# Performance work log

Hardware: AMD Instinct MI355X
Metric: run time of the kernel (lower is better)

## Reference

```python
import jax, jax.numpy as jnp
import numpy as np

N_LAYERS, D_MODEL, H, D_K, D_V, D_FF, VOCAB = 6, 512, 8, 64, 64, 2048, 32000
B, S = 4, 512
NEG_INF = -jnp.inf


def positional_encoding(seq_len, d_model):
    # Faithful to the (buggy-vs-paper) source: angle = pos / 10000**(2*i/d_model),
    # sin for even i, cos for odd i (i is the raw channel index).
    pos = jnp.arange(seq_len, dtype=jnp.float32)[:, None]
    i = jnp.arange(d_model, dtype=jnp.float32)[None, :]
    angle = pos / jnp.power(10000.0, 2.0 * i / d_model)
    return jnp.where((jnp.arange(d_model) % 2 == 0)[None, :], jnp.sin(angle), jnp.cos(angle))


def layer_norm(x, g, b, eps=1e-5):
    mu = jnp.mean(x, -1, keepdims=True)
    var = jnp.mean((x - mu) ** 2, -1, keepdims=True)
    return (x - mu) * jax.lax.rsqrt(var + eps) * g + b


def mha(q_in, k_in, v_in, wq, wk, wv, wo, q_mask, k_mask, causal):
    # wq/wk: (H, D, D_K), wv: (H, D, D_V), wo: (H*D_V, D)
    q = jnp.einsum('bsd,hdk->bhsk', q_in, wq)
    k = jnp.einsum('btd,hdk->bhtk', k_in, wk)
    v = jnp.einsum('btd,hdk->bhtk', v_in, wv)
    scores = jnp.einsum('bhsk,bhtk->bhst', q, k) / jnp.sqrt(jnp.float32(D_K))
    allowed = q_mask[:, None, :, None] & k_mask[:, None, None, :]  # (B,1,S,T)
    if causal:
        sl, tl = q_in.shape[1], k_in.shape[1]
        allowed = allowed & (jnp.arange(tl)[None, :] <= jnp.arange(sl)[:, None])[None, None]
    scores = jnp.where(allowed, scores, NEG_INF)
    attn = jax.nn.softmax(scores, axis=-1)
    out = jnp.einsum('bhst,bhtk->bshk', attn, v)  # (B,S,H,D_V)
    out = out.reshape(out.shape[0], out.shape[1], H * D_V)
    return out @ wo


def ffn(x, w1, b1, w2, b2):
    return jax.nn.relu(x @ w1 + b1) @ w2 + b2


def setup_inputs() -> dict:
    key = jax.random.key(0)
    ks = iter(jax.random.split(key, 40))
    f = lambda shape, scale: (jax.random.normal(next(ks), shape, dtype=jnp.float32) * scale)
    inp = {
        'src_tokens': jax.random.randint(next(ks), (B, S), 0, VOCAB),
        'tgt_tokens': jax.random.randint(next(ks), (B, S), 0, VOCAB),
        'src_mask': jnp.ones((B, S), dtype=bool),
        'tgt_mask': jnp.ones((B, S), dtype=bool),
        'embed': f((VOCAB, D_MODEL), 0.02),
        'enc_wqkv': f((N_LAYERS, 3, H, D_MODEL, D_K), 0.04),
        'enc_wo': f((N_LAYERS, H * D_V, D_MODEL), 0.04),
        'enc_ff_w1': f((N_LAYERS, D_MODEL, D_FF), 0.02),
        'enc_ff_b1': jnp.zeros((N_LAYERS, D_FF), jnp.float32),
        'enc_ff_w2': f((N_LAYERS, D_FF, D_MODEL), 0.02),
        'enc_ff_b2': jnp.zeros((N_LAYERS, D_MODEL), jnp.float32),
        'enc_ln_g': jnp.ones((N_LAYERS, 2, D_MODEL), jnp.float32),
        'enc_ln_b': jnp.zeros((N_LAYERS, 2, D_MODEL), jnp.float32),
        'dec_wqkv1': f((N_LAYERS, 3, H, D_MODEL, D_K), 0.04),
        'dec_wo1': f((N_LAYERS, H * D_V, D_MODEL), 0.04),
        'dec_wqkv2': f((N_LAYERS, 3, H, D_MODEL, D_K), 0.04),
        'dec_wo2': f((N_LAYERS, H * D_V, D_MODEL), 0.04),
        'dec_ff_w1': f((N_LAYERS, D_MODEL, D_FF), 0.02),
        'dec_ff_b1': jnp.zeros((N_LAYERS, D_FF), jnp.float32),
        'dec_ff_w2': f((N_LAYERS, D_FF, D_MODEL), 0.02),
        'dec_ff_b2': jnp.zeros((N_LAYERS, D_MODEL), jnp.float32),
        'dec_ln_g': jnp.ones((N_LAYERS, 3, D_MODEL), jnp.float32),
        'dec_ln_b': jnp.zeros((N_LAYERS, 3, D_MODEL), jnp.float32),
        'out_w': f((D_MODEL, VOCAB), 0.02),
        'out_b': jnp.zeros((VOCAB,), jnp.float32),
    }
    return inp


def reference(src_tokens, tgt_tokens, src_mask, tgt_mask, embed,
              enc_wqkv, enc_wo, enc_ff_w1, enc_ff_b1, enc_ff_w2, enc_ff_b2, enc_ln_g, enc_ln_b,
              dec_wqkv1, dec_wo1, dec_wqkv2, dec_wo2, dec_ff_w1, dec_ff_b1, dec_ff_w2, dec_ff_b2,
              dec_ln_g, dec_ln_b, out_w, out_b):
    pe = positional_encoding(src_tokens.shape[1], D_MODEL)
    x = embed[src_tokens] + pe[None]
    for i in range(N_LAYERS):
        a = mha(x, x, x, enc_wqkv[i, 0], enc_wqkv[i, 1], enc_wqkv[i, 2], enc_wo[i], src_mask, src_mask, False)
        x = layer_norm(x + a, enc_ln_g[i, 0], enc_ln_b[i, 0])
        x = layer_norm(x + ffn(x, enc_ff_w1[i], enc_ff_b1[i], enc_ff_w2[i], enc_ff_b2[i]), enc_ln_g[i, 1], enc_ln_b[i, 1])
    pe_t = positional_encoding(tgt_tokens.shape[1], D_MODEL)
    y = embed[tgt_tokens] + pe_t[None]
    for i in range(N_LAYERS):
        a = mha(y, y, y, dec_wqkv1[i, 0], dec_wqkv1[i, 1], dec_wqkv1[i, 2], dec_wo1[i], tgt_mask, tgt_mask, True)
        y = layer_norm(y + a, dec_ln_g[i, 0], dec_ln_b[i, 0])
        a = mha(y, x, x, dec_wqkv2[i, 0], dec_wqkv2[i, 1], dec_wqkv2[i, 2], dec_wo2[i], tgt_mask, src_mask, False)
        y = layer_norm(y + a, dec_ln_g[i, 1], dec_ln_b[i, 1])
        y = layer_norm(y + ffn(y, dec_ff_w1[i], dec_ff_b1[i], dec_ff_w2[i], dec_ff_b2[i]), dec_ln_g[i, 2], dec_ln_b[i, 2])
    return y @ out_w + out_b
```

## Files before the change

### kernel.cpp

```cpp
#include <hip/hip_runtime.h>
#include <math.h>


typedef unsigned short u16;
typedef __attribute__((ext_vector_type(8))) short short8;
typedef __attribute__((ext_vector_type(4))) float f32x4;

__device__ __forceinline__ u16 f2bf(float f){
  unsigned u = __float_as_uint(f);
  return (u16)((u + 0x7fffu + ((u >> 16) & 1u)) >> 16);
}

#define GLDS16(gp, lp) __builtin_amdgcn_global_load_lds( \
    (const __attribute__((address_space(1))) unsigned int*)(const void*)(gp), \
    (__attribute__((address_space(3))) unsigned int*)(void*)(lp), 16, 0, 0)

__global__ __launch_bounds__(256) void embed_dual_kernel(
    const int* __restrict__ src, const int* __restrict__ tgt,
    const float* __restrict__ emb,
    float* __restrict__ xb, u16* __restrict__ xh,
    float* __restrict__ yb, u16* __restrict__ yh)
{
  int which = blockIdx.x >> 11;
  int row = blockIdx.x & 2047;
  int s = row & 511;
  int t = which ? tgt[row] : src[row];
  float* out = which ? yb : xb;
  u16*  outh = which ? yh : xh;
  #pragma unroll
  for (int j = 0; j < 2; j++){
    int d = threadIdx.x + 256*j;
    float ang = (float)s * powf(10000.0f, -2.0f*(float)d/512.0f);
    float pe = (d & 1) ? cosf(ang) : sinf(ang);
    float v = emb[(size_t)t*512 + d] + pe;
    out[(size_t)row*512 + d] = v;
    outh[(size_t)row*512 + d] = f2bf(v);
  }
}

struct WDesc { const float* W; unsigned long long gs, ds; u16* dst; int K; int nx; int end; };
struct WPack { WDesc d[6]; };

__device__ __forceinline__ void cast_body(const WPack& P, int nseg, int blk){
  __shared__ u16 T[64][65];
  int s = 0;
  while (s < nseg-1 && blk >= P.d[s].end) s++;
  WDesc D = P.d[s];
  int base = s ? P.d[s-1].end : 0;
  int lb = blk - base;
  int g = lb % D.nx, kt = lb / D.nx;
  int tid = threadIdx.x;
  const float* Wb = D.W + (size_t)g*D.gs + (size_t)kt*64*D.ds;
  #pragma unroll
  for (int i = 0; i < 16; i++){
    int li = tid + 256*i;
    int kk = li >> 6, c = li & 63;
    T[kk][c] = f2bf(Wb[(size_t)kk*D.ds + c]);
  }
  __syncthreads();
  #pragma unroll
  for (int i = 0; i < 16; i++){
    int lo = tid + 256*i;
    int c = lo >> 6, kk = lo & 63;
    D.dst[(size_t)(g*64 + c)*D.K + kt*64 + kk] = T[kk][c];
  }
}

__global__ __launch_bounds__(256) void wcast_multi(WPack P, int nseg){
  cast_body(P, nseg, blockIdx.x);
}

__device__ __forceinline__ void ln_body(
    float* __restrict__ x, const float* __restrict__ res,
    const float* __restrict__ g, const float* __restrict__ bt,
    u16* __restrict__ xh, int blk)
{
  int tid = threadIdx.x, lane = tid & 63, wv = tid >> 6;
  int row = blk*4 + wv;
  size_t base = (size_t)row*512;
  float v[8]; float sum = 0.f;
  #pragma unroll
  for (int j = 0; j < 8; j++){
    int d = lane + 64*j;
    v[j] = x[base + d] + res[base + d];
    sum += v[j];
  }
  #pragma unroll
  for (int o = 32; o; o >>= 1) sum += __shfl_xor(sum, o);
  float mu = sum * (1.0f/512.0f);
  float vs = 0.f;
  #pragma unroll
  for (int j = 0; j < 8; j++){ float dd = v[j] - mu; vs += dd*dd; }
  #pragma unroll
  for (int o = 32; o; o >>= 1) vs += __shfl_xor(vs, o);
  float rstd = rsqrtf(vs*(1.0f/512.0f) + 1e-5f);
  #pragma unroll
  for (int j = 0; j < 8; j++){
    int d = lane + 64*j;
    float ov = (v[j] - mu)*rstd*g[d] + bt[d];
    x[base + d] = ov;
    xh[base + d] = f2bf(ov);
  }
}

__global__ __launch_bounds__(256) void ln_cast_kernel(
    float* __restrict__ x, const float* __restrict__ res,
    const float* __restrict__ g, const float* __restrict__ bt,
    u16* __restrict__ xh, WPack P, int nseg)
{
  int bid = blockIdx.x;
  if (bid < 512){ ln_body(x, res, g, bt, xh, bid); return; }
  cast_body(P, nseg, bid - 512);
}

__global__ __launch_bounds__(256) void ln_kernel(
    float* __restrict__ x, const float* __restrict__ res,
    const float* __restrict__ g, const float* __restrict__ bt,
    u16* __restrict__ xh)
{
  ln_body(x, res, g, bt, xh, blockIdx.x);
}

__global__ __launch_bounds__(512) void flash_attn_kernel(
    const u16* __restrict__ qkv, const u16* __restrict__ vT,
    u16* __restrict__ ctx, int causal)
{
  __shared__ __align__(16) u16 lQ[64*64];
  __shared__ __align__(16) u16 lK[4][64*64];
  __shared__ __align__(16) u16 lV[4][64*64];
  __shared__ __align__(16) u16 lP[8][16*64];
  int tid = threadIdx.x, lane = tid & 63, w = tid >> 6;
  int g = w >> 2, wl = w & 3;
  int r16 = lane & 15, l4 = lane >> 4;
  int bh = blockIdx.x >> 3, qb = blockIdx.x & 7;
  int b = bh >> 3, h = bh & 7;
  const u16* qbase = qkv + (size_t)b*512*1536 + h*64;
  int sr = tid >> 3, sc = tid & 7;

  GLDS16(qbase + (size_t)(qb*64 + sr)*1536 + ((sc ^ (sr & 7))*8),
         lQ + (w << 6)*8);
  auto stageK = [&](int buf, int tt){
    GLDS16(qbase + 512 + (size_t)(tt*64 + sr)*1536 + ((sc ^ (sr & 7))*8),
           lK[buf] + (w << 6)*8);
  };
  auto stageV = [&](int buf, int tt){
    GLDS16(vT + ((size_t)bh*64 + sr)*512 + tt*64 + ((sc ^ (sr & 7))*8),
           lV[buf] + (w << 6)*8);
  };

  int ntl = causal ? (qb + 1) : 8;
  int nrounds = (ntl + 1) >> 1;
  stageK(0, 0); stageV(0, 0);
  if (ntl > 1){ stageK(1, 1); stageV(1, 1); }
  __syncthreads();

  short8 qa[2];
  #pragma unroll
  for (int kt = 0; kt < 2; kt++){
    int q = wl*16 + r16;
    qa[kt] = *(const short8*)&lQ[q*64 + (((kt*4 + l4) ^ (q & 7))*8)];
  }

  f32x4 o[4];
  float mrow[4], lrow[4];
  #pragma unroll
  for (int j = 0; j < 4; j++){ o[j] = (f32x4){0.f,0.f,0.f,0.f}; mrow[j] = -3e38f; lrow[j] = 0.f; }

  for (int rd = 0; rd < nrounds; rd++){
    if (rd > 0) __syncthreads();
    if (rd + 1 < nrounds){
      int base = ((rd + 1) & 1)*2;
      int t0 = 2*(rd + 1);
      stageK(base, t0); stageV(base, t0);
      if (t0 + 1 < ntl){ stageK(base + 1, t0 + 1); stageV(base + 1, t0 + 1); }
    }
    int tr = 2*rd + g;
    if (tr < ntl){
      int buf = (rd & 1)*2 + g;
      f32x4 s[4];
      #pragma unroll
      for (int ct = 0; ct < 4; ct++) s[ct] = (f32x4){0.f,0.f,0.f,0.f};
      __builtin_amdgcn_s_setprio(1);
      #pragma unroll
      for (int kt = 0; kt < 2; kt++){
        #pragma unroll
        for (int ct = 0; ct < 4; ct++){
          int trow = ct*16 + r16;
          short8 kb = *(const short8*)&lK[buf][trow*64 + (((kt*4 + l4) ^ (trow & 7))*8)];
          s[ct] = __builtin_amdgcn_mfma_f32_16x16x32_bf16(qa[kt], kb, s[ct], 0, 0, 0);
        }
      }
      __builtin_amdgcn_s_setprio(0);
      float p[4][4];
      #pragma unroll
      for (int ct = 0; ct < 4; ct++)
        #pragma unroll
        for (int r = 0; r < 4; r++){
          float v = s[ct][r] * 0.125f;
          if (causal && tr == qb && (ct*16 + r16) > (wl*16 + l4*4 + r)) v = -1e30f;
          p[ct][r] = v;
        }
      #pragma unroll
      for (int r = 0; r < 4; r++){
        float pm = fmaxf(fmaxf(p[0][r], p[1][r]), fmaxf(p[2][r], p[3][r]));
        #pragma unroll
        for (int off = 1; off < 16; off <<= 1) pm = fmaxf(pm, __shfl_xor(pm, off));
        float mn = fmaxf(mrow[r], pm);
        float scl = __expf(mrow[r] - mn);
        mrow[r] = mn;
        float rs = 0.f;
        #pragma unroll
        for (int ct = 0; ct < 4; ct++){ p[ct][r] = __expf(p[ct][r] - mn); rs += p[ct][r]; }
        #pragma unroll
        for (int off = 1; off < 16; off <<= 1) rs += __shfl_xor(rs, off);
        lrow[r] = lrow[r]*scl + rs;
        #pragma unroll
        for (int jf = 0; jf < 4; jf++) o[jf][r] *= scl;
      }
      u16* myP = &lP[w][0];
      #pragma unroll
      for (int ct = 0; ct < 4; ct++)
        #pragma unroll
        for (int r = 0; r < 4; r++){
          int q = l4*4 + r, t = ct*16 + r16;
          myP[q*64 + (((t >> 3) ^ (q & 7))*8) + (t & 7)] = f2bf(p[ct][r]);
        }
      __builtin_amdgcn_s_setprio(1);
      #pragma unroll
      for (int kt = 0; kt < 2; kt++){
        short8 pa = *(const short8*)&myP[r16*64 + (((kt*4 + l4) ^ (r16 & 7))*8)];
        #pragma unroll
        for (int jf = 0; jf < 4; jf++){
          int dr = jf*16 + r16;
          short8 vv = *(const short8*)&lV[buf][dr*64 + (((kt*4 + l4) ^ (dr & 7))*8)];
          o[jf] = __builtin_amdgcn_mfma_f32_16x16x32_bf16(pa, vv, o[jf], 0, 0, 0);
        }
      }
      __builtin_amdgcn_s_setprio(0);
    }
  }

  __syncthreads();
  float* mrg = (float*)&lK[0][0];
  if (w >= 4){
    float* p = mrg + ((size_t)(wl*64 + lane))*25;
    #pragma unroll
    for (int r = 0; r < 4; r++){ p[r] = mrow[r]; p[4 + r] = lrow[r]; }
    #pragma unroll
    for (int jf = 0; jf < 4; jf++)
      #pragma unroll
      for (int r = 0; r < 4; r++) p[8 + jf*4 + r] = o[jf][r];
  }
  __syncthreads();
  if (w < 4){
    float* p = mrg + ((size_t)(w*64 + lane))*25;
    #pragma unroll
    for (int r = 0; r < 4; r++){
      float m1 = p[r], l1 = p[4 + r];
      float M  = fmaxf(mrow[r], m1);
      float s0 = __expf(mrow[r] - M), s1 = __expf(m1 - M);
      float L  = lrow[r]*s0 + l1*s1;
      float inv = 1.0f / L;
      int q = qb*64 + w*16 + l4*4 + r;
      u16* dst = ctx + (size_t)(b*512 + q)*512 + h*64;
      #pragma unroll
      for (int jf = 0; jf < 4; jf++)
        dst[jf*16 + r16] = f2bf((o[jf][r]*s0 + p[8 + jf*4 + r]*s1) * inv);
    }
  }
}

template<int BM, int BN, int WM, int WN, int WK, int VOUT, int SWZ>
__global__ __launch_bounds__(WM*WN*WK*64) void mfma_gemm(
    const u16* __restrict__ A, int lda,
    const u16* __restrict__ B, int ldb,
    void* __restrict__ C, int ldc, int cbf,
    const float* __restrict__ bias, int relu, int K, u16* __restrict__ vt)
{
  constexpr int NWC = WM*WN;
  constexpr int NT  = NWC*WK*64;
  constexpr int TPS = NWC*64;
  constexpr int SM  = BM/WM, SN = BN/WN;
  constexpr int FM  = SM/16, FN = SN/16;
  constexpr int RPS = TPS/8;
  constexpr int AG  = BM/RPS, BG = BN/RPS;
  __shared__ __align__(16) u16 lds[2][WK][(BM+BN)*64];
  int bx, by;
  if constexpr (SWZ){
    int nwg = gridDim.x * gridDim.y;
    int lin = blockIdx.y * gridDim.x + blockIdx.x;
    int q = nwg >> 3, r = nwg & 7;
    int xcd = lin & 7, idx = lin >> 3;
    int wgid = (xcd < r ? xcd*(q+1) : r*(q+1) + (xcd-r)*q) + idx;
    bx = wgid / gridDim.y; by = wgid % gridDim.y;
  } else { bx = blockIdx.x; by = blockIdx.y; }
  int tid = threadIdx.x, lane = tid & 63, w = tid >> 6;
  int wk = w / NWC, wl = w % NWC;
  int wm = wl / WN, wn = wl % WN;
  int r16 = lane & 15, l4 = lane >> 4;
  int stid = tid % TPS, slc = tid / TPS;
  int ws = stid >> 6;
  int sr = stid >> 3, sc = stid & 7;
  int scs = sc ^ (sr & 7);
  int kslc = K/WK;
  const u16* Ab = A + (size_t)by*BM*lda + (size_t)sr*lda + scs*8 + (size_t)slc*kslc;
  const u16* Bb = B + (size_t)bx*BN*ldb + (size_t)sr*ldb + scs*8 + (size_t)slc*kslc;
  f32x4 acc[FM][FN];
  #pragma unroll
  for (int i = 0; i < FM; i++)
    #pragma unroll
    for (int j = 0; j < FN; j++)
      acc[i][j] = (f32x4){0.f, 0.f, 0.f, 0.f};

  auto stage = [&](int buf, int kt){
    #pragma unroll
    for (int s = 0; s < AG; s++)
      GLDS16(Ab + (size_t)(s*RPS)*lda + kt, &lds[buf][slc][(s*RPS + (ws << 3))*64]);
    #pragma unroll
    for (int s = 0; s < BG; s++)
      GLDS16(Bb + (size_t)(s*RPS)*ldb + kt, &lds[buf][slc][(BM + s*RPS + (ws << 3))*64]);
  };
  stage(0, 0);
  int nk = kslc >> 6, cur = 0;
  for (int kt = 0; kt < nk; kt++){
    __syncthreads();
    if (kt + 1 < nk) stage(cur ^ 1, (kt + 1) << 6);
    #pragma unroll
    for (int ks = 0; ks < 2; ks++){
      short8 av[FM], bv[FN];
      #pragma unroll
      for (int i = 0; i < FM; i++){
        int row = wm*SM + i*16 + r16;
        av[i] = *(const short8*)&lds[cur][wk][row*64 + (((ks*4 + l4) ^ (row & 7))*8)];
      }
      #pragma unroll
      for (int j = 0; j < FN; j++){
        int row = wn*SN + j*16 + r16;
        bv[j] = *(const short8*)&lds[cur][wk][(BM + row)*64 + (((ks*4 + l4) ^ (row & 7))*8)];
      }
      #pragma unroll
      for (int i = 0; i < FM; i++)
        #pragma unroll
        for (int j = 0; j < FN; j++)
          acc[i][j] = __builtin_amdgcn_mfma_f32_16x16x32_bf16(av[i], bv[j], acc[i][j], 0, 0, 0);
    }
    cur ^= 1;
  }

  if constexpr (WK == 2){
    __syncthreads();
    float* Mg = (float*)&lds[0][0][0];
    if (wk == 1){
      #pragma unroll
      for (int i = 0; i < FM; i++)
        #pragma unroll
        for (int j = 0; j < FN; j++)
          #pragma unroll
          for (int r = 0; r < 4; r++)
            Mg[(size_t)(wm*SM + i*16 + l4*4 + r)*(BN + 4) + wn*SN + j*16 + r16]
                = acc[i][j][r];
    }
    __syncthreads();
    if (wk == 0){
      #pragma unroll
      for (int i = 0; i < FM; i++)
        #pragma unroll
        for (int j = 0; j < FN; j++)
          #pragma unroll
          for (int r = 0; r < 4; r++)
            acc[i][j][r] += Mg[(size_t)(wm*SM + i*16 + l4*4 + r)*(BN + 4)
                               + wn*SN + j*16 + r16];
    }
  }

  if constexpr (VOUT){
    int nblk = bx * BN;
    if (nblk >= 1024){
      constexpr int TP = BM + 4;
      u16* T = &lds[0][0][0];
      __syncthreads();
      if (wk == 0){
        #pragma unroll
        for (int i = 0; i < FM; i++){
          int t0 = wm*SM + i*16 + l4*4;
          #pragma unroll
          for (int j = 0; j < FN; j++){
            int d = wn*SN + j*16 + r16;
            unsigned q01 = (unsigned)f2bf(acc[i][j][0]) | ((unsigned)f2bf(acc[i][j][1]) << 16);
            unsigned q23 = (unsigned)f2bf(acc[i][j][2]) | ((unsigned)f2bf(acc[i][j][3]) << 16);
            uint2 pk; pk.x = q01; pk.y = q23;
            *(uint2*)&T[d*TP + t0] = pk;
          }
        }
      }
      __syncthreads();
      int h0 = (nblk - 1024) >> 6;
      int b = (by * BM) >> 9;
      int t0g = (by * BM) & 511;
      constexpr int U2PR = BM/4;
      constexpr int NIT = (BN*BM)/(NT*4);
      #pragma unroll
      for (int it = 0; it < NIT; it++){
        int idx = it*NT + tid;
        int d = idx / U2PR, tq = (idx % U2PR)*4;
        int hh = d >> 6, dd = d & 63;
        *(uint2*)&vt[((size_t)((b*8 + h0 + hh)*64 + dd))*512 + t0g + tq] =
            *(const uint2*)&T[d*TP + tq];
      }
      return;
    }
  }

  if (wk != 0) return;
  int m0 = by*BM + wm*SM, n0 = bx*BN + wn*SN;
  int r4 = l4*4;
  #pragma unroll
  for (int i = 0; i < FM; i++){
    #pragma unroll
    for (int j = 0; j < FN; j++){
      int col = n0 + j*16 + r16;
      float bi = bias ? bias[col] : 0.f;
      #pragma unroll
      for (int r = 0; r < 4; r++){
        int rowg = m0 + i*16 + r4 + r;
        float o = acc[i][j][r] + bi;
        if (relu) o = fmaxf(o, 0.f);
        if (cbf) ((u16*)C)[(size_t)rowg*ldc + col] = f2bf(o);
        else     ((float*)C)[(size_t)rowg*ldc + col] = o;
      }
    }
  }
}

__global__ __launch_bounds__(256) void xattn_qkv_gemm(
    const u16* __restrict__ Ay, const u16* __restrict__ Ax,
    const u16* __restrict__ Bt, u16* __restrict__ C, u16* __restrict__ vt)
{
  constexpr int BM=64, BN=64, WM=2, WN=2, NT=256;
  constexpr int SM=BM/WM, SN=BN/WN, FM=SM/16, FN=SN/16, RPS=NT/8;
  constexpr int AG=BM/RPS, BG=BN/RPS;
  __shared__ __align__(16) u16 lA[2][BM*64];
  __shared__ __align__(16) u16 lB[2][BN*64];
  int tid = threadIdx.x, lane = tid & 63, w = tid >> 6;
  int wm = w / WN, wn = w % WN;
  int r16 = lane & 15, l4 = lane >> 4;
  int sr = (w << 3) + (lane >> 3);
  int sc = lane & 7;
  int scs = sc ^ (sr & 7);
  int z = blockIdx.z;
  const u16* A = (z == 0) ? Ay : Ax;
  const u16* Ab = A + (size_t)blockIdx.y*BM*512 + (size_t)sr*512 + scs*8;
  const u16* Bb = Bt + (size_t)(z*512 + blockIdx.x*BN)*512 + (size_t)sr*512 + scs*8;
  f32x4 acc[FM][FN];
  #pragma unroll
  for (int i = 0; i < FM; i++)
    #pragma unroll
    for (int j = 0; j < FN; j++)
      acc[i][j] = (f32x4){0.f, 0.f, 0.f, 0.f};
  auto stage = [&](int buf, int kt){
    #pragma unroll
    for (int s = 0; s < AG; s++)
      GLDS16(Ab + (size_t)(s*RPS)*512 + kt, &lA[buf][(s*RPS + (w << 3))*64]);
    #pragma unroll
    for (int s = 0; s < BG; s++)
      GLDS16(Bb + (size_t)(s*RPS)*512 + kt, &lB[buf][(s*RPS + (w << 3))*64]);
  };
  stage(0, 0);
  int cur = 0;
  for (int kt = 0; kt < 8; kt++){
    __syncthreads();
    if (kt + 1 < 8) stage(cur ^ 1, (kt + 1) << 6);
    #pragma unroll
    for (int ks = 0; ks < 2; ks++){
      short8 av[FM], bv[FN];
      #pragma unroll
      for (int i = 0; i < FM; i++){
        int row = wm*SM + i*16 + r16;
        av[i] = *(const short8*)&lA[cur][row*64 + (((ks*4 + l4) ^ (row & 7))*8)];
      }
      #pragma unroll
      for (int j = 0; j < FN; j++){
        int row = wn*SN + j*16 + r16;
        bv[j] = *(const short8*)&lB[cur][row*64 + (((ks*4 + l4) ^ (row & 7))*8)];
      }
      #pragma unroll
      for (int i = 0; i < FM; i++)
        #pragma unroll
        for (int j = 0; j < FN; j++)
          acc[i][j] = __builtin_amdgcn_mfma_f32_16x16x32_bf16(av[i], bv[j], acc[i][j], 0, 0, 0);
    }
    cur ^= 1;
  }
  if (z == 2){
    constexpr int TP = BM + 4;
    u16* T = (u16*)&lA[0][0];
    __syncthreads();
    #pragma unroll
    for (int i = 0; i < FM; i++){
      int t0 = wm*SM + i*16 + l4*4;
      #pragma unroll
      for (int j = 0; j < FN; j++){
        int d = wn*SN + j*16 + r16;
        unsigned q01 = (unsigned)f2bf(acc[i][j][0]) | ((unsigned)f2bf(acc[i][j][1]) << 16);
        unsigned q23 = (unsigned)f2bf(acc[i][j][2]) | ((unsigned)f2bf(acc[i][j][3]) << 16);
        uint2 pk; pk.x = q01; pk.y = q23;
        *(uint2*)&T[d*TP + t0] = pk;
      }
    }
    __syncthreads();
    int h = blockIdx.x;
    int b = (blockIdx.y * BM) >> 9;
    int t0g = (blockIdx.y * BM) & 511;
    u16* dst = vt + (size_t)(b*8 + h)*64*512;
    #pragma unroll
    for (int it = 0; it < (BM*64)/(NT*4); it++){
      int idx = it*NT + tid;
      int d = idx >> 4, tq = (idx & 15)*4;
      *(uint2*)&dst[(size_t)d*512 + t0g + tq] = *(const uint2*)&T[d*TP + tq];
    }
    return;
  }
  int m0 = blockIdx.y*BM + wm*SM, n0 = z*512 + blockIdx.x*BN + wn*SN;
  int r4 = l4*4;
  #pragma unroll
  for (int i = 0; i < FM; i++)
    #pragma unroll
    for (int j = 0; j < FN; j++)
      #pragma unroll
      for (int r = 0; r < 4; r++){
        int rowg = m0 + i*16 + r4 + r;
        C[(size_t)rowg*1536 + n0 + j*16 + r16] = f2bf(acc[i][j][r]);
      }
}

extern "C" void kernel_launch(void* const* d_in, const int* in_sizes, int n_in,
                              void* d_out, int out_size, void* d_ws, size_t ws_size,
                              hipStream_t stream)
{
  (void)in_sizes; (void)n_in; (void)out_size; (void)ws_size;
  const int*   src_tok   = (const int*)  d_in[0];
  const int*   tgt_tok   = (const int*)  d_in[1];
  const float* emb       = (const float*)d_in[4];
  const float* enc_wqkv  = (const float*)d_in[5];
  const float* enc_wo    = (const float*)d_in[6];
  const float* enc_ff_w1 = (const float*)d_in[7];
  const float* enc_ff_b1 = (const float*)d_in[8];
  const float* enc_ff_w2 = (const float*)d_in[9];
  const float* enc_ff_b2 = (const float*)d_in[10];
  const float* enc_ln_g  = (const float*)d_in[11];
  const float* enc_ln_b  = (const float*)d_in[12];
  const float* dec_wqkv1 = (const float*)d_in[13];
  const float* dec_wo1   = (const float*)d_in[14];
  const float* dec_wqkv2 = (const float*)d_in[15];
  const float* dec_wo2   = (const float*)d_in[16];
  const float* dec_ff_w1 = (const float*)d_in[17];
  const float* dec_ff_b1 = (const float*)d_in[18];
  const float* dec_ff_w2 = (const float*)d_in[19];
  const float* dec_ff_b2 = (const float*)d_in[20];
  const float* dec_ln_g  = (const float*)d_in[21];
  const float* dec_ln_b  = (const float*)d_in[22];
  const float* out_w     = (const float*)d_in[23];
  const float* out_b     = (const float*)d_in[24];
  float* outp = (float*)d_out;

  const size_t MB = 1024*1024;
  char* wsb = (char*)d_ws;
  float* xb     = (float*)(wsb + 0*MB);
  u16*   sQKV2  = (u16*)  (wsb + 0*MB);
  u16*   sWO2   = (u16*)  (wsb + 1*MB + 512*1024);
  float* yb     = (float*)(wsb + 4*MB);
  u16*   xh     = (u16*)  (wsb + 8*MB);
  u16*   ctxb   = (u16*)  (wsb + 10*MB);
  u16*   yh     = (u16*)  (wsb + 12*MB);
  u16*   qkvb   = (u16*)  (wsb + 14*MB);
  u16*   vT     = (u16*)  (wsb + 20*MB);
  u16*   hid    = (u16*)  (wsb + 14*MB);
  u16*   sQKV   = (u16*)  (wsb + 22*MB);
  u16*   sWO    = (u16*)  (wsb + 23*MB + 512*1024);
  u16*   sFF1   = (u16*)  (wsb + 24*MB);
  u16*   sFF2   = (u16*)  (wsb + 26*MB);
  float* proj   = (float*)(wsb + 28*MB);
  u16*   wvbuf  = (u16*)  (wsb + 14*MB);

  auto g64 = [&](const u16* A,int lda,const u16* B,int ldb,void* C,int ldc,
                 int cbf,const float* bias,int relu,int M,int N,int K){
    mfma_gemm<64,64,2,2,2,0,0><<<dim3(N/64, M/64), 512, 0, stream>>>(
        A,lda,B,ldb,C,ldc,cbf,bias,relu,K,nullptr);
  };
  auto g128 = [&](const u16* A,int lda,const u16* B,int ldb,void* C,int ldc,
                  int cbf,const float* bias,int relu,int M,int N,int K){
    mfma_gemm<128,128,2,2,2,0,0><<<dim3(N/128, M/128), 512, 0, stream>>>(
        A,lda,B,ldb,C,ldc,cbf,bias,relu,K,nullptr);
  };
  auto gvocab = [&](const u16* A,const u16* B,void* C,int ldc,
                    const float* bias,int N){
    mfma_gemm<128,64,2,2,1,0,1><<<dim3(N/64, 16), 256, 0, stream>>>(
        A,512,B,512,C,ldc,0,bias,0,512,nullptr);
  };
  auto gqkv = [&](const u16* A,const u16* B,u16* C,u16* vt){
    mfma_gemm<128,128,2,2,2,1,0><<<dim3(12, 16), 512, 0, stream>>>(
        A,512,B,512,C,1536,1,nullptr,0,512,vt);
  };
  auto ln = [&](float* x, const float* g, const float* b, u16* oh){
    ln_kernel<<<512, 256, 0, stream>>>(x, proj, g, b, oh);
  };
  auto packof = [&](WDesc* segs, int n, int& tot){
    WPack P; tot = 0;
    for (int s = 0; s < n; s++){
      tot += segs[s].nx * (segs[s].K/64);
      segs[s].end = tot;
      P.d[s] = segs[s];
    }
    for (int s = n; s < 6; s++) P.d[s] = P.d[0];
    return P;
  };
  auto cast = [&](WDesc* segs, int n){
    int tot; WPack P = packof(segs, n, tot);
    wcast_multi<<<tot, 256, 0, stream>>>(P, n);
  };
  auto ln_cast = [&](float* x, const float* g, const float* b, u16* oh,
                     WDesc* segs, int n){
    int tot; WPack P = packof(segs, n, tot);
    ln_cast_kernel<<<512 + tot, 256, 0, stream>>>(x, proj, g, b, oh, P, n);
  };

  const size_t WQKV_L = (size_t)3*8*512*64;
  auto enc_segs = [&](int i, WDesc* s){
    s[0] = {enc_wqkv + i*WQKV_L,            32768, 64,   sQKV, 512,  24, 0};
    s[1] = {enc_wo   + (size_t)i*262144,    64,    512,  sWO,  512,  8,  0};
    s[2] = {enc_ff_w1+ (size_t)i*512*2048,  64,    2048, sFF1, 512,  32, 0};
    s[3] = {enc_ff_w2+ (size_t)i*2048*512,  64,    512,  sFF2, 2048, 8,  0};
  };
  auto dec_segs = [&](int i, WDesc* s){
    s[0] = {dec_wqkv1 + i*WQKV_L,           32768, 64,   sQKV,  512,  24, 0};
    s[1] = {dec_wo1   + (size_t)i*262144,   64,    512,  sWO,   512,  8,  0};
    s[2] = {dec_ff_w1 + (size_t)i*512*2048, 64,    2048, sFF1,  512,  32, 0};
    s[3] = {dec_ff_w2 + (size_t)i*2048*512, 64,    512,  sFF2,  2048, 8,  0};
    s[4] = {dec_wqkv2 + i*WQKV_L,           32768, 64,   sQKV2, 512,  24, 0};
    s[5] = {dec_wo2   + (size_t)i*262144,   64,    512,  sWO2,  512,  8,  0};
  };

  embed_dual_kernel<<<4096, 256, 0, stream>>>(src_tok, tgt_tok, emb, xb, xh, yb, yh);

  { WDesc s[4]; enc_segs(0, s); cast(s, 4); }
  for (int i = 0; i < 6; i++){
    gqkv(xh, sQKV, qkvb, vT);
    flash_attn_kernel<<<256, 512, 0, stream>>>(qkvb, vT, ctxb, 0);
    g64(ctxb, 512, sWO, 512, proj, 512, 0, nullptr, 0, 2048, 512, 512);
    ln(xb, enc_ln_g + i*1024, enc_ln_b + i*1024, xh);
    g128(xh, 512, sFF1, 512, hid, 2048, 1, enc_ff_b1 + i*2048, 1, 2048, 2048, 512);
    g64(hid, 2048, sFF2, 2048, proj, 512, 0, enc_ff_b2 + i*512, 0, 2048, 512, 2048);
    if (i < 5){
      WDesc s[4]; enc_segs(i+1, s);
      ln_cast(xb, enc_ln_g + i*1024 + 512, enc_ln_b + i*1024 + 512, xh, s, 4);
    } else {
      ln(xb, enc_ln_g + i*1024 + 512, enc_ln_b + i*1024 + 512, xh);
    }
  }

  { WDesc s[6]; dec_segs(0, s); cast(s, 6); }
  for (int i = 0; i < 6; i++){
    gqkv(yh, sQKV, qkvb, vT);
    flash_attn_kernel<<<256, 512, 0, stream>>>(qkvb, vT, ctxb, 1);
    g64(ctxb, 512, sWO, 512, proj, 512, 0, nullptr, 0, 2048, 512, 512);
    ln(yb, dec_ln_g + i*1536,        dec_ln_b + i*1536,        yh);
    xattn_qkv_gemm<<<dim3(8, 32, 3), 256, 0, stream>>>(yh, xh, sQKV2, qkvb, vT);
    flash_attn_kernel<<<256, 512, 0, stream>>>(qkvb, vT, ctxb, 0);
    g64(ctxb, 512, sWO2, 512, proj, 512, 0, nullptr, 0, 2048, 512, 512);
    ln(yb, dec_ln_g + i*1536 + 512,  dec_ln_b + i*1536 + 512,  yh);
    g128(yh, 512, sFF1, 512, hid, 2048, 1, dec_ff_b1 + i*2048, 1, 2048, 2048, 512);
    g64(hid, 2048, sFF2, 2048, proj, 512, 0, dec_ff_b2 + i*512, 0, 2048, 512, 2048);
    if (i < 5){
      WDesc s[6]; dec_segs(i+1, s);
      ln_cast(yb, dec_ln_g + i*1536 + 1024, dec_ln_b + i*1536 + 1024, yh, s, 6);
    } else {
      ln(yb, dec_ln_g + i*1536 + 1024, dec_ln_b + i*1536 + 1024, yh);
    }
  }

  for (int c = 0; c < 2; c++){
    int c0 = c*16000;
    WDesc seg[1] = {{out_w + c0, 64, 32000, wvbuf, 512, 250, 0}};
    cast(seg, 1);
    gvocab(yh, wvbuf, outp + c0, 32000, out_b + c0, 16000);
  }
}
```

Baseline: 1.298 ms.

## Split-K across two warp groups in cross-attn QKV GEMM; share Q/P LDS in flash attention

```diff
diff --git a/kernel.cpp b/kernel.cpp
--- a/kernel.cpp
+++ b/kernel.cpp
@@ -125,10 +125,9 @@
     const u16* __restrict__ qkv, const u16* __restrict__ vT,
     u16* __restrict__ ctx, int causal)
 {
-  __shared__ __align__(16) u16 lQ[64*64];
+  __shared__ __align__(16) u16 lQP[8*16*64];
   __shared__ __align__(16) u16 lK[4][64*64];
   __shared__ __align__(16) u16 lV[4][64*64];
-  __shared__ __align__(16) u16 lP[8][16*64];
   int tid = threadIdx.x, lane = tid & 63, w = tid >> 6;
   int g = w >> 2, wl = w & 3;
   int r16 = lane & 15, l4 = lane >> 4;
@@ -138,7 +137,7 @@
   int sr = tid >> 3, sc = tid & 7;
 
   GLDS16(qbase + (size_t)(qb*64 + sr)*1536 + ((sc ^ (sr & 7))*8),
-         lQ + (w << 6)*8);
+         lQP + (w << 6)*8);
   auto stageK = [&](int buf, int tt){
     GLDS16(qbase + 512 + (size_t)(tt*64 + sr)*1536 + ((sc ^ (sr & 7))*8),
            lK[buf] + (w << 6)*8);
@@ -158,8 +157,9 @@
   #pragma unroll
   for (int kt = 0; kt < 2; kt++){
     int q = wl*16 + r16;
-    qa[kt] = *(const short8*)&lQ[q*64 + (((kt*4 + l4) ^ (q & 7))*8)];
-  }
+    qa[kt] = *(const short8*)&lQP[q*64 + (((kt*4 + l4) ^ (q & 7))*8)];
+  }
+  __syncthreads();
 
   f32x4 o[4];
   float mrow[4], lrow[4];
@@ -217,7 +217,7 @@
         #pragma unroll
         for (int jf = 0; jf < 4; jf++) o[jf][r] *= scl;
       }
-      u16* myP = &lP[w][0];
+      u16* myP = &lQP[w*16*64];
       #pragma unroll
       for (int ct = 0; ct < 4; ct++)
         #pragma unroll
@@ -432,25 +432,28 @@
   }
 }
 
-__global__ __launch_bounds__(256) void xattn_qkv_gemm(
+__global__ __launch_bounds__(512) void xattn_qkv_gemm(
     const u16* __restrict__ Ay, const u16* __restrict__ Ax,
     const u16* __restrict__ Bt, u16* __restrict__ C, u16* __restrict__ vt)
 {
-  constexpr int BM=64, BN=64, WM=2, WN=2, NT=256;
-  constexpr int SM=BM/WM, SN=BN/WN, FM=SM/16, FN=SN/16, RPS=NT/8;
+  constexpr int BM=64, BN=64, WM=2, WN=2, WK=2;
+  constexpr int NWC=WM*WN, NT=NWC*WK*64, TPS=NWC*64;
+  constexpr int SM=BM/WM, SN=BN/WN, FM=SM/16, FN=SN/16, RPS=TPS/8;
   constexpr int AG=BM/RPS, BG=BN/RPS;
-  __shared__ __align__(16) u16 lA[2][BM*64];
-  __shared__ __align__(16) u16 lB[2][BN*64];
+  __shared__ __align__(16) u16 lds[2][WK][(BM+BN)*64];
   int tid = threadIdx.x, lane = tid & 63, w = tid >> 6;
-  int wm = w / WN, wn = w % WN;
+  int wk = w / NWC, wl = w % NWC;
+  int wm = wl / WN, wn = wl % WN;
   int r16 = lane & 15, l4 = lane >> 4;
-  int sr = (w << 3) + (lane >> 3);
-  int sc = lane & 7;
+  int stid = tid % TPS, slc = tid / TPS;
+  int ws = stid >> 6;
+  int sr = stid >> 3, sc = stid & 7;
   int scs = sc ^ (sr & 7);
   int z = blockIdx.z;
   const u16* A = (z == 0) ? Ay : Ax;
-  const u16* Ab = A + (size_t)blockIdx.y*BM*512 + (size_t)sr*512 + scs*8;
-  const u16* Bb = Bt + (size_t)(z*512 + blockIdx.x*BN)*512 + (size_t)sr*512 + scs*8;
+  const u16* Ab = A + (size_t)blockIdx.y*BM*512 + (size_t)sr*512 + scs*8 + (size_t)slc*256;
+  const u16* Bb = Bt + (size_t)(z*512 + blockIdx.x*BN)*512 + (size_t)sr*512 + scs*8
+                  + (size_t)slc*256;
   f32x4 acc[FM][FN];
   #pragma unroll
   for (int i = 0; i < FM; i++)
@@ -460,28 +463,28 @@
   auto stage = [&](int buf, int kt){
     #pragma unroll
     for (int s = 0; s < AG; s++)
-      GLDS16(Ab + (size_t)(s*RPS)*512 + kt, &lA[buf][(s*RPS + (w << 3))*64]);
+      GLDS16(Ab + (size_t)(s*RPS)*512 + kt, &lds[buf][slc][(s*RPS + (ws << 3))*64]);
     #pragma unroll
     for (int s = 0; s < BG; s++)
-      GLDS16(Bb + (size_t)(s*RPS)*512 + kt, &lB[buf][(s*RPS + (w << 3))*64]);
+      GLDS16(Bb + (size_t)(s*RPS)*512 + kt, &lds[buf][slc][(BM + s*RPS + (ws << 3))*64]);
   };
   stage(0, 0);
   int cur = 0;
-  for (int kt = 0; kt < 8; kt++){
+  for (int kt = 0; kt < 4; kt++){
     __syncthreads();
-    if (kt + 1 < 8) stage(cur ^ 1, (kt + 1) << 6);
+    if (kt + 1 < 4) stage(cur ^ 1, (kt + 1) << 6);
     #pragma unroll
     for (int ks = 0; ks < 2; ks++){
       short8 av[FM], bv[FN];
       #pragma unroll
       for (int i = 0; i < FM; i++){
         int row = wm*SM + i*16 + r16;
-        av[i] = *(const short8*)&lA[cur][row*64 + (((ks*4 + l4) ^ (row & 7))*8)];
+        av[i] = *(const short8*)&lds[cur][wk][row*64 + (((ks*4 + l4) ^ (row & 7))*8)];
       }
       #pragma unroll
       for (int j = 0; j < FN; j++){
         int row = wn*SN + j*16 + r16;
-        bv[j] = *(const short8*)&lB[cur][row*64 + (((ks*4 + l4) ^ (row & 7))*8)];
+        bv[j] = *(const short8*)&lds[cur][wk][(BM + row)*64 + (((ks*4 + l4) ^ (row & 7))*8)];
       }
       #pragma unroll
       for (int i = 0; i < FM; i++)
@@ -491,20 +494,45 @@
     }
     cur ^= 1;
   }
+  __syncthreads();
+  float* Mg = (float*)&lds[0][0][0];
+  if (wk == 1){
+    #pragma unroll
+    for (int i = 0; i < FM; i++)
+      #pragma unroll
+      for (int j = 0; j < FN; j++)
+        #pragma unroll
+        for (int r = 0; r < 4; r++)
+          Mg[(size_t)(wm*SM + i*16 + l4*4 + r)*(BN + 4) + wn*SN + j*16 + r16]
+              = acc[i][j][r];
+  }
+  __syncthreads();
+  if (wk == 0){
+    #pragma unroll
+    for (int i = 0; i < FM; i++)
+      #pragma unroll
+      for (int j = 0; j < FN; j++)
+        #pragma unroll
+        for (int r = 0; r < 4; r++)
+          acc[i][j][r] += Mg[(size_t)(wm*SM + i*16 + l4*4 + r)*(BN + 4)
+                             + wn*SN + j*16 + r16];
+  }
   if (z == 2){
     constexpr int TP = BM + 4;
-    u16* T = (u16*)&lA[0][0];
+    u16* T = &lds[0][0][0];
     __syncthreads();
-    #pragma unroll
-    for (int i = 0; i < FM; i++){
-      int t0 = wm*SM + i*16 + l4*4;
-      #pragma unroll
-      for (int j = 0; j < FN; j++){
-        int d = wn*SN + j*16 + r16;
-        unsigned q01 = (unsigned)f2bf(acc[i][j][0]) | ((unsigned)f2bf(acc[i][j][1]) << 16);
-        unsigned q23 = (unsigned)f2bf(acc[i][j][2]) | ((unsigned)f2bf(acc[i][j][3]) << 16);
-        uint2 pk; pk.x = q01; pk.y = q23;
-        *(uint2*)&T[d*TP + t0] = pk;
+    if (wk == 0){
+      #pragma unroll
+      for (int i = 0; i < FM; i++){
+        int t0 = wm*SM + i*16 + l4*4;
+        #pragma unroll
+        for (int j = 0; j < FN; j++){
+          int d = wn*SN + j*16 + r16;
+          unsigned q01 = (unsigned)f2bf(acc[i][j][0]) | ((unsigned)f2bf(acc[i][j][1]) << 16);
+          unsigned q23 = (unsigned)f2bf(acc[i][j][2]) | ((unsigned)f2bf(acc[i][j][3]) << 16);
+          uint2 pk; pk.x = q01; pk.y = q23;
+          *(uint2*)&T[d*TP + t0] = pk;
+        }
       }
     }
     __syncthreads();
@@ -520,6 +548,7 @@
     }
     return;
   }
+  if (wk != 0) return;
   int m0 = blockIdx.y*BM + wm*SM, n0 = z*512 + blockIdx.x*BN + wn*SN;
   int r4 = l4*4;
   #pragma unroll
@@ -664,7 +693,7 @@
     flash_attn_kernel<<<256, 512, 0, stream>>>(qkvb, vT, ctxb, 1);
     g64(ctxb, 512, sWO, 512, proj, 512, 0, nullptr, 0, 2048, 512, 512);
     ln(yb, dec_ln_g + i*1536,        dec_ln_b + i*1536,        yh);
-    xattn_qkv_gemm<<<dim3(8, 32, 3), 256, 0, stream>>>(yh, xh, sQKV2, qkvb, vT);
+    xattn_qkv_gemm<<<dim3(8, 32, 3), 512, 0, stream>>>(yh, xh, sQKV2, qkvb, vT);
     flash_attn_kernel<<<256, 512, 0, stream>>>(qkvb, vT, ctxb, 0);
     g64(ctxb, 512, sWO2, 512, proj, 512, 0, nullptr, 0, 2048, 512, 512);
     ln(yb, dec_ln_g + i*1536 + 512,  dec_ln_b + i*1536 + 512,  yh);
```

Result: no change. 1.299 ms (+0.1%).
